# Kernel optimization log

Measured on AMD Instinct MI355X. Metric: run time of the kernel, lower is better.

## Reference

```python
import jax, jax.numpy as jnp
import numpy as np

N = 4096      # num nodes
D = 256       # hidden_dim
H = 4         # num attention heads (separate single-head MHA modules)
E = 131072    # num edges
EPS = 1e-5


def setup_inputs() -> dict:
    key = jax.random.key(0)
    ks = jax.random.split(key, 12)
    s = 0.02
    x = jax.random.normal(ks[0], (N, D), dtype=jnp.float32)
    edge_index = jax.random.randint(ks[1], (2, E), 0, N, dtype=jnp.int64)
    # per-head in_proj split into q/k/v, stacked over heads [H, D, D]
    Wq = jax.random.normal(ks[2], (H, D, D), dtype=jnp.float32) * s
    Wk = jax.random.normal(ks[3], (H, D, D), dtype=jnp.float32) * s
    Wv = jax.random.normal(ks[4], (H, D, D), dtype=jnp.float32) * s
    bq = jnp.zeros((H, D), dtype=jnp.float32)
    bk = jnp.zeros((H, D), dtype=jnp.float32)
    bv = jnp.zeros((H, D), dtype=jnp.float32)
    Wo = jax.random.normal(ks[5], (H, D, D), dtype=jnp.float32) * s  # per-head MHA out_proj
    bo = jnp.zeros((H, D), dtype=jnp.float32)
    Wp = jax.random.normal(ks[6], (D, H * D), dtype=jnp.float32) * s  # output_projection
    bp = jnp.zeros((D,), dtype=jnp.float32)
    gamma = jnp.ones((D,), dtype=jnp.float32)
    beta = jnp.zeros((D,), dtype=jnp.float32)
    return dict(x=x, edge_index=edge_index, Wq=Wq, bq=bq, Wk=Wk, bk=bk,
                Wv=Wv, bv=bv, Wo=Wo, bo=bo, Wp=Wp, bp=bp, gamma=gamma, beta=beta)


def _build_mask(edge_index, n):
    row, col = edge_index[0], edge_index[1]
    mask = jnp.full((n, n), -jnp.inf, dtype=jnp.float32)
    mask = mask.at[row, col].set(0.0)
    mask = mask.at[col, row].set(0.0)
    mask = mask.at[jnp.arange(n), jnp.arange(n)].set(0.0)
    return mask


def reference(x, edge_index, Wq, bq, Wk, bk, Wv, bv, Wo, bo, Wp, bp, gamma, beta):
    mask = _build_mask(edge_index, x.shape[0])  # [N, N] additive, -inf on non-edges
    # per-head projections (torch Linear: x @ W.T + b); h = head axis
    q = jnp.einsum('nd,hed->hne', x, Wq) + bq[:, None, :]
    k = jnp.einsum('nd,hed->hne', x, Wk) + bk[:, None, :]
    v = jnp.einsum('nd,hed->hne', x, Wv) + bv[:, None, :]
    scores = jnp.einsum('hne,hme->hnm', q, k) / jnp.sqrt(jnp.float32(D)) + mask[None]
    attn = jax.nn.softmax(scores, axis=-1)                    # [H, N, N]
    o = jnp.einsum('hnm,hme->hne', attn, v)                   # [H, N, D]
    head_out = jnp.einsum('hne,hfe->hnf', o, Wo) + bo[:, None, :]  # per-head out_proj
    concatenated = jnp.transpose(head_out, (1, 0, 2)).reshape(x.shape[0], H * D)
    out = concatenated @ Wp.T + bp                             # [N, D]
    mu = jnp.mean(out, axis=-1, keepdims=True)
    var = jnp.mean(jnp.square(out - mu), axis=-1, keepdims=True)
    return (out - mu) / jnp.sqrt(var + EPS) * gamma + beta
```

## Files before the change

kernel.cpp:

```cpp
#include <hip/hip_runtime.h>
#include <hip/hip_bf16.h>

#define N_NODES 4096
#define DIM 256
#define NHEAD 4
#define NEDGE 131072
#define MWORDS 128
#define MAXDEG 192
#define GBK 64
#define MASK_BLOCKS 528

typedef unsigned short ushort_t;
typedef __attribute__((ext_vector_type(8))) short short8;
typedef __attribute__((ext_vector_type(4))) float f32x4;

__device__ __forceinline__ ushort_t f2bf(float f) {
    unsigned u = __float_as_uint(f);
    unsigned r = u + 0x7FFFu + ((u >> 16) & 1u);
    return (ushort_t)(r >> 16);
}
__device__ __forceinline__ float bf2f(ushort_t u) {
    return __uint_as_float((unsigned)u << 16);
}

__global__ __launch_bounds__(256) void init_kernel(
    const int* __restrict__ ei, unsigned* __restrict__ mask,
    const float* __restrict__ x,  const float* __restrict__ Wq,
    const float* __restrict__ Wk, const float* __restrict__ Wv,
    const float* __restrict__ Wo, const float* __restrict__ Wp,
    ushort_t* __restrict__ xb, ushort_t* __restrict__ wstack,
    ushort_t* __restrict__ wob, ushort_t* __restrict__ wpb) {
    const int bid = blockIdx.x;
    if (bid < MASK_BLOCKS) {
        const int t = bid * 256 + threadIdx.x;
        if (t < NEDGE) {
            const int r = ei[t] & (N_NODES - 1);
            const int c = ei[NEDGE + t] & (N_NODES - 1);
            atomicOr(&mask[r * MWORDS + (c >> 5)], 1u << (c & 31));
            atomicOr(&mask[c * MWORDS + (r >> 5)], 1u << (r & 31));
        } else if (t < NEDGE + N_NODES) {
            const int i = t - NEDGE;
            atomicOr(&mask[i * MWORDS + (i >> 5)], 1u << (i & 31));
        }
        return;
    }
    const int e = ((bid - MASK_BLOCKS) * 256 + threadIdx.x) << 2;
    const float* src; ushort_t* dst; int off;
    if (e < 1048576)      { src = x;  dst = xb;              off = e; }
    else if (e < 1310720) { src = Wq; dst = wstack;          off = e - 1048576; }
    else if (e < 1572864) { src = Wk; dst = wstack + 262144; off = e - 1310720; }
    else if (e < 1835008) { src = Wv; dst = wstack + 524288; off = e - 1572864; }
    else if (e < 2097152) { src = Wo; dst = wob;             off = e - 1835008; }
    else                  { src = Wp; dst = wpb;             off = e - 2097152; }
    const float4 v = *(const float4*)(src + off);
    ushort4 r;
    r.x = f2bf(v.x); r.y = f2bf(v.y); r.z = f2bf(v.z); r.w = f2bf(v.w);
    *(ushort4*)(dst + off) = r;
}

template <int MODE>
__global__ __launch_bounds__(256) void mfma_gemm_kernel(
    const ushort_t* __restrict__ Wb, const ushort_t* __restrict__ Xb,
    const float* __restrict__ b0, const float* __restrict__ b1,
    const float* __restrict__ b2,
    ushort_t* __restrict__ qb, ushort_t* __restrict__ kvh,
    void* __restrict__ outp, int K) {
    __shared__ ushort_t Wt[128][GBK + 8];
    __shared__ ushort_t Xt[128][GBK + 8];
    const int tid = threadIdx.x;
    const int lane = tid & 63;
    const int wid = tid >> 6;
    const int wr = wid >> 1, wc = wid & 1;
    const int zoff = (MODE == 1) ? blockIdx.z : 0;
    const ushort_t* Wp_ = Wb + (size_t)zoff * (256 * 256);
    const ushort_t* Xp_ = Xb + (size_t)zoff * ((size_t)N_NODES * 256);
    const int chB = blockIdx.x * 128;
    const int ndB = blockIdx.y * 128;

    f32x4 acc[4][4] = {};

    for (int kt = 0; kt < K; kt += GBK) {
        short8 wreg[4], xreg[4];
#pragma unroll
        for (int i = 0; i < 4; ++i) {
            const int flat = tid + (i << 8);
            const int r = flat >> 3, s = flat & 7;
            wreg[i] = *(const short8*)(Wp_ + (size_t)(chB + r) * K + kt + (s << 3));
            xreg[i] = *(const short8*)(Xp_ + (size_t)(ndB + r) * K + kt + (s << 3));
        }
        __syncthreads();
#pragma unroll
        for (int i = 0; i < 4; ++i) {
            const int flat = tid + (i << 8);
            const int r = flat >> 3, s = flat & 7;
            *(short8*)&Wt[r][s << 3] = wreg[i];
            *(short8*)&Xt[r][s << 3] = xreg[i];
        }
        __syncthreads();
#pragma unroll
        for (int kk = 0; kk < 2; ++kk) {
            short8 af[4], bf[4];
            const int ko = (kk << 5) + ((lane >> 4) << 3);
#pragma unroll
            for (int m = 0; m < 4; ++m)
                af[m] = *(const short8*)&Wt[wr * 64 + m * 16 + (lane & 15)][ko];
#pragma unroll
            for (int n = 0; n < 4; ++n)
                bf[n] = *(const short8*)&Xt[wc * 64 + n * 16 + (lane & 15)][ko];
#pragma unroll
            for (int m = 0; m < 4; ++m)
#pragma unroll
                for (int n = 0; n < 4; ++n)
                    acc[m][n] = __builtin_amdgcn_mfma_f32_16x16x32_bf16(
                        af[m], bf[n], acc[m][n], 0, 0, 0);
        }
    }

    const int lhi = lane >> 4;
    const int llo = lane & 15;
    int op = 0, h = 0;
    if (MODE == 0) { op = chB >> 10; h = (chB >> 8) & 3; }
#pragma unroll
    for (int m = 0; m < 4; ++m) {
        const int ch = chB + wr * 64 + m * 16 + (lhi << 2);
        float4 bia;
        if (MODE == 0) {
            const float* bb = (op == 0 ? b0 : op == 1 ? b1 : b2) + (h << 8);
            bia = *(const float4*)&bb[ch & 255];
        } else {
            bia = *(const float4*)&b0[(zoff << 8) + ch];
        }
#pragma unroll
        for (int n = 0; n < 4; ++n) {
            const int node = ndB + wc * 64 + n * 16 + llo;
            const float v0 = acc[m][n][0] + bia.x;
            const float v1 = acc[m][n][1] + bia.y;
            const float v2 = acc[m][n][2] + bia.z;
            const float v3 = acc[m][n][3] + bia.w;
            ushort4 r;
            r.x = f2bf(v0); r.y = f2bf(v1); r.z = f2bf(v2); r.w = f2bf(v3);
            if (MODE == 1) {
                *(ushort4*)&((ushort_t*)outp)[(size_t)node * 1024 + (zoff << 8) + ch] = r;
            } else {
                const int c = ch & 255;
                if (op == 0)
                    *(ushort4*)&qb[(((size_t)h * N_NODES + node) << 8) + c] = r;
                else if (op == 1)
                    *(ushort4*)&kvh[(((size_t)h * N_NODES + node) << 9) + c] = r;
                else
                    *(ushort4*)&kvh[(((size_t)h * N_NODES + node) << 9) + 256 + c] = r;
            }
        }
    }
}

__global__ __launch_bounds__(256) void final_ln_kernel(
    const ushort_t* __restrict__ Wb,
    const ushort_t* __restrict__ Xb,
    const float* __restrict__ bp,
    const float* __restrict__ gamma, const float* __restrict__ beta,
    float* __restrict__ out) {
    __shared__ ushort_t Wt[256][GBK + 8];
    __shared__ ushort_t Xt[64][GBK + 8];
    __shared__ float redS[4][64];
    __shared__ float redQ[4][64];
    const int tid = threadIdx.x;
    const int lane = tid & 63;
    const int wid = tid >> 6;
    const int ndB = blockIdx.x * 64;

    f32x4 acc[4][4] = {};

    for (int kt = 0; kt < 1024; kt += GBK) {
        short8 wreg[8], xreg[2];
#pragma unroll
        for (int i = 0; i < 8; ++i) {
            const int flat = tid + (i << 8);
            const int r = flat >> 3, s = flat & 7;
            wreg[i] = *(const short8*)(Wb + (size_t)r * 1024 + kt + (s << 3));
        }
#pragma unroll
        for (int i = 0; i < 2; ++i) {
            const int flat = tid + (i << 8);
            const int r = flat >> 3, s = flat & 7;
            xreg[i] = *(const short8*)(Xb + (size_t)(ndB + r) * 1024 + kt + (s << 3));
        }
        __syncthreads();
#pragma unroll
        for (int i = 0; i < 8; ++i) {
            const int flat = tid + (i << 8);
            const int r = flat >> 3, s = flat & 7;
            *(short8*)&Wt[r][s << 3] = wreg[i];
        }
#pragma unroll
        for (int i = 0; i < 2; ++i) {
            const int flat = tid + (i << 8);
            const int r = flat >> 3, s = flat & 7;
            *(short8*)&Xt[r][s << 3] = xreg[i];
        }
        __syncthreads();
#pragma unroll
        for (int kk = 0; kk < 2; ++kk) {
            short8 af[4], bf[4];
            const int ko = (kk << 5) + ((lane >> 4) << 3);
#pragma unroll
            for (int m = 0; m < 4; ++m)
                af[m] = *(const short8*)&Wt[wid * 64 + m * 16 + (lane & 15)][ko];
#pragma unroll
            for (int n = 0; n < 4; ++n)
                bf[n] = *(const short8*)&Xt[n * 16 + (lane & 15)][ko];
#pragma unroll
            for (int m = 0; m < 4; ++m)
#pragma unroll
                for (int n = 0; n < 4; ++n)
                    acc[m][n] = __builtin_amdgcn_mfma_f32_16x16x32_bf16(
                        af[m], bf[n], acc[m][n], 0, 0, 0);
        }
    }

    const int lhi = lane >> 4;
    const int llo = lane & 15;
    float vout[4][4][4];
    float psum[4] = {0.f, 0.f, 0.f, 0.f};
    float psq[4]  = {0.f, 0.f, 0.f, 0.f};
#pragma unroll
    for (int m = 0; m < 4; ++m) {
        const int f0 = wid * 64 + m * 16 + (lhi << 2);
        const float4 bia = *(const float4*)&bp[f0];
#pragma unroll
        for (int n = 0; n < 4; ++n) {
            const float v0 = acc[m][n][0] + bia.x;
            const float v1 = acc[m][n][1] + bia.y;
            const float v2 = acc[m][n][2] + bia.z;
            const float v3 = acc[m][n][3] + bia.w;
            vout[m][n][0] = v0; vout[m][n][1] = v1;
            vout[m][n][2] = v2; vout[m][n][3] = v3;
            psum[n] += v0 + v1 + v2 + v3;
            psq[n]  += v0 * v0 + v1 * v1 + v2 * v2 + v3 * v3;
        }
    }
#pragma unroll
    for (int n = 0; n < 4; ++n) {
        psum[n] += __shfl_xor(psum[n], 16);
        psum[n] += __shfl_xor(psum[n], 32);
        psq[n]  += __shfl_xor(psq[n], 16);
        psq[n]  += __shfl_xor(psq[n], 32);
    }
    if (lhi == 0) {
#pragma unroll
        for (int n = 0; n < 4; ++n) {
            redS[wid][n * 16 + llo] = psum[n];
            redQ[wid][n * 16 + llo] = psq[n];
        }
    }
    __syncthreads();
    float mean[4], inv[4];
#pragma unroll
    for (int n = 0; n < 4; ++n) {
        const int nd = n * 16 + llo;
        const float S = redS[0][nd] + redS[1][nd] + redS[2][nd] + redS[3][nd];
        const float Q = redQ[0][nd] + redQ[1][nd] + redQ[2][nd] + redQ[3][nd];
        const float mu = S * (1.0f / DIM);
        const float var = Q * (1.0f / DIM) - mu * mu;
        mean[n] = mu;
        inv[n] = 1.0f / sqrtf(var + 1e-5f);
    }
#pragma unroll
    for (int m = 0; m < 4; ++m) {
        const int f0 = wid * 64 + m * 16 + (lhi << 2);
        const float4 gv = *(const float4*)&gamma[f0];
        const float4 bv = *(const float4*)&beta[f0];
#pragma unroll
        for (int n = 0; n < 4; ++n) {
            const int node = ndB + n * 16 + llo;
            float4 r;
            r.x = (vout[m][n][0] - mean[n]) * inv[n] * gv.x + bv.x;
            r.y = (vout[m][n][1] - mean[n]) * inv[n] * gv.y + bv.y;
            r.z = (vout[m][n][2] - mean[n]) * inv[n] * gv.z + bv.z;
            r.w = (vout[m][n][3] - mean[n]) * inv[n] * gv.w + bv.w;
            *(float4*)&out[(size_t)node * DIM + f0] = r;
        }
    }
}

__global__ __launch_bounds__(256) void attn_sparse_kernel(const unsigned* __restrict__ mask,
                                                          const ushort_t* __restrict__ qb,
                                                          const ushort_t* __restrict__ kvh,
                                                          ushort_t* __restrict__ ob) {
    __shared__ int nbr[4][MAXDEG];
    const int tid = threadIdx.x;
    const int w = tid >> 6;
    const int lane = tid & 63;
    const int xcd = blockIdx.x & 7;
    const int h = xcd >> 1;
    const int node = ((xcd & 1) << 11) + ((blockIdx.x >> 3) << 2) + w;

    const unsigned m0 = mask[node * MWORDS + lane];
    const unsigned m1 = mask[node * MWORDS + 64 + lane];
    const int c = __popc(m0) + __popc(m1);
    int s = c;
#pragma unroll
    for (int d = 1; d < 64; d <<= 1) {
        const int t = __shfl_up(s, d);
        if (lane >= d) s += t;
    }
    const int deg0 = __shfl(s, 63);
    const int deg = deg0 < MAXDEG ? deg0 : MAXDEG;
    int pos = s - c;
    unsigned mm = m0;
    int bj = lane << 5;
    while (mm) {
        const int b = __ffs(mm) - 1; mm &= mm - 1;
        if (pos < MAXDEG) nbr[w][pos] = bj + b;
        ++pos;
    }
    mm = m1; bj = (lane + 64) << 5;
    while (mm) {
        const int b = __ffs(mm) - 1; mm &= mm - 1;
        if (pos < MAXDEG) nbr[w][pos] = bj + b;
        ++pos;
    }
    __syncthreads();

    const int sub = lane >> 4;
    const int sl = lane & 15;

    const ushort_t* qp = qb + (((size_t)h * N_NODES + node) << 8) + (sl << 4);
    const short8 q0 = *(const short8*)qp;
    const short8 q1 = *(const short8*)(qp + 8);
    float qf[16];
#pragma unroll
    for (int i = 0; i < 8; ++i) {
        qf[i] = bf2f((ushort_t)q0[i]);
        qf[8 + i] = bf2f((ushort_t)q1[i]);
    }
    float oa[16];
#pragma unroll
    for (int i = 0; i < 16; ++i) oa[i] = 0.f;
    float denom = 0.f;

    const ushort_t* kbase = kvh + (((size_t)h * N_NODES) << 9) + (sl << 4);
    const float SC = 0.0625f * 1.44269504f;

    for (int n0 = 0; n0 < deg; n0 += 4) {
        const int idx = n0 + sub;
        const bool valid = idx < deg;
        const int j = nbr[w][valid ? idx : 0];
        const ushort_t* kp = kbase + ((size_t)j << 9);
        const short8 k0 = *(const short8*)kp;
        const short8 k1 = *(const short8*)(kp + 8);
        const short8 v0 = *(const short8*)(kp + 256);
        const short8 v1 = *(const short8*)(kp + 264);
        float p = 0.f;
#pragma unroll
        for (int i = 0; i < 8; ++i)
            p += qf[i] * bf2f((ushort_t)k0[i]) + qf[8 + i] * bf2f((ushort_t)k1[i]);
        p += __shfl_xor(p, 1);
        p += __shfl_xor(p, 2);
        p += __shfl_xor(p, 4);
        p += __shfl_xor(p, 8);
        const float wt = valid ? __builtin_amdgcn_exp2f(p * SC) : 0.f;
        denom += wt;
#pragma unroll
        for (int i = 0; i < 8; ++i) {
            oa[i] += wt * bf2f((ushort_t)v0[i]);
            oa[8 + i] += wt * bf2f((ushort_t)v1[i]);
        }
    }
    denom += __shfl_xor(denom, 16);
    denom += __shfl_xor(denom, 32);
#pragma unroll
    for (int i = 0; i < 16; ++i) {
        oa[i] += __shfl_xor(oa[i], 16);
        oa[i] += __shfl_xor(oa[i], 32);
    }
    if (sub == 0) {
        const float inv = 1.0f / denom;
        short8 r0, r1;
#pragma unroll
        for (int i = 0; i < 8; ++i) {
            r0[i] = (short)f2bf(oa[i] * inv);
            r1[i] = (short)f2bf(oa[8 + i] * inv);
        }
        ushort_t* op_ = ob + (((size_t)h * N_NODES + node) << 8) + (sl << 4);
        *(short8*)op_ = r0;
        *(short8*)(op_ + 8) = r1;
    }
}

extern "C" void kernel_launch(void* const* d_in, const int* in_sizes, int n_in,
                              void* d_out, int out_size, void* d_ws, size_t ws_size,
                              hipStream_t stream) {
    const float* x     = (const float*)d_in[0];
    const int*   ei    = (const int*)d_in[1];
    const float* Wq    = (const float*)d_in[2];
    const float* bq    = (const float*)d_in[3];
    const float* Wk    = (const float*)d_in[4];
    const float* bk    = (const float*)d_in[5];
    const float* Wv    = (const float*)d_in[6];
    const float* bv    = (const float*)d_in[7];
    const float* Wo    = (const float*)d_in[8];
    const float* bo    = (const float*)d_in[9];
    const float* Wp    = (const float*)d_in[10];
    const float* bp    = (const float*)d_in[11];
    const float* gamma = (const float*)d_in[12];
    const float* beta  = (const float*)d_in[13];
    float* outf = (float*)d_out;

    char* ws = (char*)d_ws;
    unsigned* mask    = (unsigned*)(ws);
    ushort_t* xb      = (ushort_t*)(ws + (size_t)( 2 << 20));
    ushort_t* qb      = (ushort_t*)(ws + (size_t)( 4 << 20));
    ushort_t* kvh     = (ushort_t*)(ws + (size_t)(12 << 20));
    ushort_t* ob      = (ushort_t*)(ws + (size_t)(28 << 20));
    ushort_t* concatb = (ushort_t*)(ws + (size_t)(36 << 20));
    ushort_t* wstack  = (ushort_t*)(ws + (size_t)(48 << 20));
    ushort_t* wob     = (ushort_t*)(ws + (size_t)(50 << 20));
    ushort_t* wpb     = (ushort_t*)(ws + (size_t)(51 << 20));

    hipMemsetAsync(mask, 0, N_NODES * MWORDS * sizeof(unsigned), stream);

    init_kernel<<<MASK_BLOCKS + 2304, 256, 0, stream>>>(
        ei, mask, x, Wq, Wk, Wv, Wo, Wp, xb, wstack, wob, wpb);

    mfma_gemm_kernel<0><<<dim3(24, 32), 256, 0, stream>>>(
        wstack, xb, bq, bk, bv, qb, kvh, nullptr, 256);

    attn_sparse_kernel<<<N_NODES, 256, 0, stream>>>(mask, qb, kvh, ob);

    mfma_gemm_kernel<1><<<dim3(2, 32, NHEAD), 256, 0, stream>>>(
        wob, ob, bo, nullptr, nullptr, nullptr, nullptr, concatb, 256);

    final_ln_kernel<<<64, 256, 0, stream>>>(wpb, concatb, bp, gamma, beta, outf);
}
```

Measured before the change: 203.9 us.

## Fold per-head out_proj into output projection and use direct global-to-LDS loads

Precomputes a combined weight Wp·Wo per head, plus a combined bias, inside the init kernel. This removes the separate per-head out_proj GEMM and its concat buffer, and the attention kernel now writes directly in the concatenated [N, 4*256] layout. The remaining GEMMs stage tiles with global_load_lds instead of register round-trips, and the LDS padding is dropped, which may add bank conflicts. The weight-fold runs in fp32 on 64 blocks with scalar loops; that adds setup work on every call and changes rounding slightly.

```diff
diff --git a/kernel.cpp b/kernel.cpp
--- a/kernel.cpp
+++ b/kernel.cpp
@@ -9,6 +9,8 @@
 #define MAXDEG 192
 #define GBK 64
 #define MASK_BLOCKS 528
+#define CONV_BLOCKS 1792
+#define PREP_BLOCKS 64
 
 typedef unsigned short ushort_t;
 typedef __attribute__((ext_vector_type(8))) short short8;
@@ -22,14 +24,19 @@
 __device__ __forceinline__ float bf2f(ushort_t u) {
     return __uint_as_float((unsigned)u << 16);
 }
+
+#define GLD16(g, l) __builtin_amdgcn_global_load_lds( \
+    (__attribute__((address_space(1))) void*)(g),     \
+    (__attribute__((address_space(3))) void*)(l), 16, 0, 0)
 
 __global__ __launch_bounds__(256) void init_kernel(
     const int* __restrict__ ei, unsigned* __restrict__ mask,
     const float* __restrict__ x,  const float* __restrict__ Wq,
     const float* __restrict__ Wk, const float* __restrict__ Wv,
     const float* __restrict__ Wo, const float* __restrict__ Wp,
+    const float* __restrict__ bo, const float* __restrict__ bp,
     ushort_t* __restrict__ xb, ushort_t* __restrict__ wstack,
-    ushort_t* __restrict__ wob, ushort_t* __restrict__ wpb) {
+    ushort_t* __restrict__ mstack, float* __restrict__ bcomb) {
     const int bid = blockIdx.x;
     if (bid < MASK_BLOCKS) {
         const int t = bid * 256 + threadIdx.x;
@@ -44,57 +51,70 @@
         }
         return;
     }
-    const int e = ((bid - MASK_BLOCKS) * 256 + threadIdx.x) << 2;
-    const float* src; ushort_t* dst; int off;
-    if (e < 1048576)      { src = x;  dst = xb;              off = e; }
-    else if (e < 1310720) { src = Wq; dst = wstack;          off = e - 1048576; }
-    else if (e < 1572864) { src = Wk; dst = wstack + 262144; off = e - 1310720; }
-    else if (e < 1835008) { src = Wv; dst = wstack + 524288; off = e - 1572864; }
-    else if (e < 2097152) { src = Wo; dst = wob;             off = e - 1835008; }
-    else                  { src = Wp; dst = wpb;             off = e - 2097152; }
-    const float4 v = *(const float4*)(src + off);
-    ushort4 r;
-    r.x = f2bf(v.x); r.y = f2bf(v.y); r.z = f2bf(v.z); r.w = f2bf(v.w);
-    *(ushort4*)(dst + off) = r;
-}
-
-template <int MODE>
-__global__ __launch_bounds__(256) void mfma_gemm_kernel(
+    if (bid < MASK_BLOCKS + CONV_BLOCKS) {
+        const int e = ((bid - MASK_BLOCKS) * 256 + threadIdx.x) << 2;
+        const float* src; ushort_t* dst; int off;
+        if (e < 1048576)      { src = x;  dst = xb;              off = e; }
+        else if (e < 1310720) { src = Wq; dst = wstack;          off = e - 1048576; }
+        else if (e < 1572864) { src = Wk; dst = wstack + 262144; off = e - 1310720; }
+        else                  { src = Wv; dst = wstack + 524288; off = e - 1572864; }
+        const float4 v = *(const float4*)(src + off);
+        ushort4 r;
+        r.x = f2bf(v.x); r.y = f2bf(v.y); r.z = f2bf(v.z); r.w = f2bf(v.w);
+        *(ushort4*)(dst + off) = r;
+        return;
+    }
+    const int pb = bid - (MASK_BLOCKS + CONV_BLOCKS);
+    const int h = pb & 3;
+    const int f0 = (pb >> 2) << 4;
+    const int e = threadIdx.x;
+    const float* woh = Wo + (size_t)h * (DIM * DIM);
+    float acc[16];
+#pragma unroll
+    for (int f = 0; f < 16; ++f) acc[f] = 0.f;
+    for (int d = 0; d < 256; ++d) {
+        const float wv = woh[d * 256 + e];
+#pragma unroll
+        for (int f = 0; f < 16; ++f)
+            acc[f] += Wp[(size_t)(f0 + f) * 1024 + (h << 8) + d] * wv;
+    }
+#pragma unroll
+    for (int f = 0; f < 16; ++f)
+        mstack[(size_t)(f0 + f) * 1024 + (h << 8) + e] = f2bf(acc[f]);
+    if (e < 16) {
+        float s = (h == 0) ? bp[f0 + e] : 0.f;
+        for (int d = 0; d < 256; ++d)
+            s += Wp[(size_t)(f0 + e) * 1024 + (h << 8) + d] * bo[(h << 8) + d];
+        atomicAdd(&bcomb[f0 + e], s);
+    }
+}
+
+__global__ __launch_bounds__(256) void qkv_gemm_kernel(
     const ushort_t* __restrict__ Wb, const ushort_t* __restrict__ Xb,
-    const float* __restrict__ b0, const float* __restrict__ b1,
-    const float* __restrict__ b2,
-    ushort_t* __restrict__ qb, ushort_t* __restrict__ kvh,
-    void* __restrict__ outp, int K) {
-    __shared__ ushort_t Wt[128][GBK + 8];
-    __shared__ ushort_t Xt[128][GBK + 8];
+    const float* __restrict__ bq, const float* __restrict__ bk,
+    const float* __restrict__ bv,
+    ushort_t* __restrict__ qb, ushort_t* __restrict__ kvh) {
+    __shared__ ushort_t Wt[128][GBK];
+    __shared__ ushort_t Xt[128][GBK];
     const int tid = threadIdx.x;
     const int lane = tid & 63;
     const int wid = tid >> 6;
     const int wr = wid >> 1, wc = wid & 1;
-    const int zoff = (MODE == 1) ? blockIdx.z : 0;
-    const ushort_t* Wp_ = Wb + (size_t)zoff * (256 * 256);
-    const ushort_t* Xp_ = Xb + (size_t)zoff * ((size_t)N_NODES * 256);
     const int chB = blockIdx.x * 128;
     const int ndB = blockIdx.y * 128;
+    const int K = 256;
 
     f32x4 acc[4][4] = {};
 
     for (int kt = 0; kt < K; kt += GBK) {
-        short8 wreg[4], xreg[4];
-#pragma unroll
-        for (int i = 0; i < 4; ++i) {
-            const int flat = tid + (i << 8);
-            const int r = flat >> 3, s = flat & 7;
-            wreg[i] = *(const short8*)(Wp_ + (size_t)(chB + r) * K + kt + (s << 3));
-            xreg[i] = *(const short8*)(Xp_ + (size_t)(ndB + r) * K + kt + (s << 3));
-        }
         __syncthreads();
 #pragma unroll
-        for (int i = 0; i < 4; ++i) {
-            const int flat = tid + (i << 8);
-            const int r = flat >> 3, s = flat & 7;
-            *(short8*)&Wt[r][s << 3] = wreg[i];
-            *(short8*)&Xt[r][s << 3] = xreg[i];
+        for (int c = 0; c < 4; ++c) {
+            const int r0 = (wid << 5) + (c << 3);
+            GLD16(Wb + (size_t)(chB + r0 + (lane >> 3)) * K + kt + ((lane & 7) << 3),
+                  &Wt[r0][0]);
+            GLD16(Xb + (size_t)(ndB + r0 + (lane >> 3)) * K + kt + ((lane & 7) << 3),
+                  &Xt[r0][0]);
         }
         __syncthreads();
 #pragma unroll
@@ -118,38 +138,28 @@
 
     const int lhi = lane >> 4;
     const int llo = lane & 15;
-    int op = 0, h = 0;
-    if (MODE == 0) { op = chB >> 10; h = (chB >> 8) & 3; }
+    const int op = chB >> 10;
+    const int h = (chB >> 8) & 3;
 #pragma unroll
     for (int m = 0; m < 4; ++m) {
         const int ch = chB + wr * 64 + m * 16 + (lhi << 2);
-        float4 bia;
-        if (MODE == 0) {
-            const float* bb = (op == 0 ? b0 : op == 1 ? b1 : b2) + (h << 8);
-            bia = *(const float4*)&bb[ch & 255];
-        } else {
-            bia = *(const float4*)&b0[(zoff << 8) + ch];
-        }
+        const float* bb = (op == 0 ? bq : op == 1 ? bk : bv) + (h << 8);
+        const float4 bia = *(const float4*)&bb[ch & 255];
 #pragma unroll
         for (int n = 0; n < 4; ++n) {
             const int node = ndB + wc * 64 + n * 16 + llo;
-            const float v0 = acc[m][n][0] + bia.x;
-            const float v1 = acc[m][n][1] + bia.y;
-            const float v2 = acc[m][n][2] + bia.z;
-            const float v3 = acc[m][n][3] + bia.w;
             ushort4 r;
-            r.x = f2bf(v0); r.y = f2bf(v1); r.z = f2bf(v2); r.w = f2bf(v3);
-            if (MODE == 1) {
-                *(ushort4*)&((ushort_t*)outp)[(size_t)node * 1024 + (zoff << 8) + ch] = r;
-            } else {
-                const int c = ch & 255;
-                if (op == 0)
-                    *(ushort4*)&qb[(((size_t)h * N_NODES + node) << 8) + c] = r;
-                else if (op == 1)
-                    *(ushort4*)&kvh[(((size_t)h * N_NODES + node) << 9) + c] = r;
-                else
-                    *(ushort4*)&kvh[(((size_t)h * N_NODES + node) << 9) + 256 + c] = r;
-            }
+            r.x = f2bf(acc[m][n][0] + bia.x);
+            r.y = f2bf(acc[m][n][1] + bia.y);
+            r.z = f2bf(acc[m][n][2] + bia.z);
+            r.w = f2bf(acc[m][n][3] + bia.w);
+            const int c = ch & 255;
+            if (op == 0)
+                *(ushort4*)&qb[(((size_t)h * N_NODES + node) << 8) + c] = r;
+            else if (op == 1)
+                *(ushort4*)&kvh[(((size_t)h * N_NODES + node) << 9) + c] = r;
+            else
+                *(ushort4*)&kvh[(((size_t)h * N_NODES + node) << 9) + 256 + c] = r;
         }
     }
 }
@@ -157,11 +167,11 @@
 __global__ __launch_bounds__(256) void final_ln_kernel(
     const ushort_t* __restrict__ Wb,
     const ushort_t* __restrict__ Xb,
-    const float* __restrict__ bp,
+    const float* __restrict__ bcomb,
     const float* __restrict__ gamma, const float* __restrict__ beta,
     float* __restrict__ out) {
-    __shared__ ushort_t Wt[256][GBK + 8];
-    __shared__ ushort_t Xt[64][GBK + 8];
+    __shared__ ushort_t Wt[256][GBK];
+    __shared__ ushort_t Xt[64][GBK];
     __shared__ float redS[4][64];
     __shared__ float redQ[4][64];
     const int tid = threadIdx.x;
@@ -172,31 +182,18 @@
     f32x4 acc[4][4] = {};
 
     for (int kt = 0; kt < 1024; kt += GBK) {
-        short8 wreg[8], xreg[2];
-#pragma unroll
-        for (int i = 0; i < 8; ++i) {
-            const int flat = tid + (i << 8);
-            const int r = flat >> 3, s = flat & 7;
-            wreg[i] = *(const short8*)(Wb + (size_t)r * 1024 + kt + (s << 3));
-        }
-#pragma unroll
-        for (int i = 0; i < 2; ++i) {
-            const int flat = tid + (i << 8);
-            const int r = flat >> 3, s = flat & 7;
-            xreg[i] = *(const short8*)(Xb + (size_t)(ndB + r) * 1024 + kt + (s << 3));
-        }
         __syncthreads();
 #pragma unroll
-        for (int i = 0; i < 8; ++i) {
-            const int flat = tid + (i << 8);
-            const int r = flat >> 3, s = flat & 7;
-            *(short8*)&Wt[r][s << 3] = wreg[i];
-        }
-#pragma unroll
-        for (int i = 0; i < 2; ++i) {
-            const int flat = tid + (i << 8);
-            const int r = flat >> 3, s = flat & 7;
-            *(short8*)&Xt[r][s << 3] = xreg[i];
+        for (int c = 0; c < 8; ++c) {
+            const int r0 = (wid << 6) + (c << 3);
+            GLD16(Wb + (size_t)(r0 + (lane >> 3)) * 1024 + kt + ((lane & 7) << 3),
+                  &Wt[r0][0]);
+        }
+#pragma unroll
+        for (int c = 0; c < 2; ++c) {
+            const int r0 = (wid << 4) + (c << 3);
+            GLD16(Xb + (size_t)(ndB + r0 + (lane >> 3)) * 1024 + kt + ((lane & 7) << 3),
+                  &Xt[r0][0]);
         }
         __syncthreads();
 #pragma unroll
@@ -226,7 +223,7 @@
 #pragma unroll
     for (int m = 0; m < 4; ++m) {
         const int f0 = wid * 64 + m * 16 + (lhi << 2);
-        const float4 bia = *(const float4*)&bp[f0];
+        const float4 bia = *(const float4*)&bcomb[f0];
 #pragma unroll
         for (int n = 0; n < 4; ++n) {
             const float v0 = acc[m][n][0] + bia.x;
@@ -382,7 +379,7 @@
             r0[i] = (short)f2bf(oa[i] * inv);
             r1[i] = (short)f2bf(oa[8 + i] * inv);
         }
-        ushort_t* op_ = ob + (((size_t)h * N_NODES + node) << 8) + (sl << 4);
+        ushort_t* op_ = ob + (size_t)node * 1024 + (h << 8) + (sl << 4);
         *(short8*)op_ = r0;
         *(short8*)(op_ + 8) = r1;
     }
@@ -408,28 +405,23 @@
     float* outf = (float*)d_out;
 
     char* ws = (char*)d_ws;
-    unsigned* mask    = (unsigned*)(ws);
-    ushort_t* xb      = (ushort_t*)(ws + (size_t)( 2 << 20));
-    ushort_t* qb      = (ushort_t*)(ws + (size_t)( 4 << 20));
-    ushort_t* kvh     = (ushort_t*)(ws + (size_t)(12 << 20));
-    ushort_t* ob      = (ushort_t*)(ws + (size_t)(28 << 20));
-    ushort_t* concatb = (ushort_t*)(ws + (size_t)(36 << 20));
-    ushort_t* wstack  = (ushort_t*)(ws + (size_t)(48 << 20));
-    ushort_t* wob     = (ushort_t*)(ws + (size_t)(50 << 20));
-    ushort_t* wpb     = (ushort_t*)(ws + (size_t)(51 << 20));
-
-    hipMemsetAsync(mask, 0, N_NODES * MWORDS * sizeof(unsigned), stream);
-
-    init_kernel<<<MASK_BLOCKS + 2304, 256, 0, stream>>>(
-        ei, mask, x, Wq, Wk, Wv, Wo, Wp, xb, wstack, wob, wpb);
-
-    mfma_gemm_kernel<0><<<dim3(24, 32), 256, 0, stream>>>(
-        wstack, xb, bq, bk, bv, qb, kvh, nullptr, 256);
+    unsigned* mask   = (unsigned*)(ws);
+    float*    bcomb  = (float*)   (ws + (size_t)( 2 << 20));
+    ushort_t* xb     = (ushort_t*)(ws + (size_t)( 4 << 20));
+    ushort_t* qb     = (ushort_t*)(ws + (size_t)( 6 << 20));
+    ushort_t* kvh    = (ushort_t*)(ws + (size_t)(14 << 20));
+    ushort_t* ob     = (ushort_t*)(ws + (size_t)(30 << 20));
+    ushort_t* wstack = (ushort_t*)(ws + (size_t)(48 << 20));
+    ushort_t* mstack = (ushort_t*)(ws + (size_t)(50 << 20));
+
+    hipMemsetAsync(ws, 0, (size_t)(2 << 20) + 1024, stream);
+
+    init_kernel<<<MASK_BLOCKS + CONV_BLOCKS + PREP_BLOCKS, 256, 0, stream>>>(
+        ei, mask, x, Wq, Wk, Wv, Wo, Wp, bo, bp, xb, wstack, mstack, bcomb);
+
+    qkv_gemm_kernel<<<dim3(24, 32), 256, 0, stream>>>(wstack, xb, bq, bk, bv, qb, kvh);
 
     attn_sparse_kernel<<<N_NODES, 256, 0, stream>>>(mask, qb, kvh, ob);
 
-    mfma_gemm_kernel<1><<<dim3(2, 32, NHEAD), 256, 0, stream>>>(
-        wob, ob, bo, nullptr, nullptr, nullptr, nullptr, concatb, 256);
-
-    final_ln_kernel<<<64, 256, 0, stream>>>(wpb, concatb, bp, gamma, beta, outf);
-}
+    final_ln_kernel<<<64, 256, 0, stream>>>(mstack, ob, bcomb, gamma, beta, outf);
+}
```

New measurement: 241.4 us. +18.4%, slower.
